# Performance work log

Measured on AMD Instinct MI355X. Metric: run time of the kernel, lower is better.

The kernel has to match this reference:

```python
import jax, jax.numpy as jnp
import numpy as np

LOG_INV_TEMP = float(np.log(1.0 / 0.07))
B, N_IMG, N_GPS, G_DIM = 256, 49, 32, 256


def setup_inputs() -> dict:
    key = jax.random.key(0)
    k1, k2 = jax.random.split(key)
    return {
        "image_g_tokens": jax.random.normal(k1, (B, N_IMG, G_DIM), dtype=jnp.float32),
        "gps_g_tokens": jax.random.normal(k2, (B, N_GPS, G_DIM), dtype=jnp.float32),
        "logit_scale": jnp.asarray(LOG_INV_TEMP, dtype=jnp.float32),
    }


def _l2norm(x, eps=1e-12):
    # matches F.normalize(p=2, dim=-1)
    n = jnp.sqrt(jnp.sum(x * x, axis=-1, keepdims=True))
    return x / jnp.maximum(n, eps)


def _ce(logits, labels):
    # mean cross-entropy with integer labels
    logz = jax.nn.logsumexp(logits, axis=1)
    picked = jnp.take_along_axis(logits, labels[:, None], axis=1)[:, 0]
    return jnp.mean(logz - picked)


def reference(image_g_tokens, gps_g_tokens, logit_scale):
    img = _l2norm(image_g_tokens)   # (B, n, d)
    gps = _l2norm(gps_g_tokens)     # (B, m, d)
    # dist not initialized -> gather is identity, global == local
    scale = jnp.minimum(jnp.exp(logit_scale), 100.0)

    # token-level max-sim: (B, G, n, m) pairwise similarities
    sims_i2g = jnp.einsum('bnd,gmd->bgnm', img, gps)
    sims_g2i = jnp.einsum('bmd,gnd->bgmn', gps, img)
    logits_i2g = jnp.mean(jnp.max(sims_i2g, axis=3), axis=2) * scale  # (B, G)
    logits_g2i = jnp.mean(jnp.max(sims_g2i, axis=3), axis=2) * scale  # (B, G)

    labels = jnp.arange(img.shape[0])
    loss = (_ce(logits_i2g, labels) + _ce(logits_g2i, labels)) / 2.0
    return loss
```

## Files before the change

kernel.cpp:

```cpp
#include <hip/hip_runtime.h>

#define BB   256
#define NIMG 49
#define NGPS 32
#define DIM  256
#define MPAD 64

typedef __attribute__((ext_vector_type(8))) __bf16 bf16x8;
typedef __attribute__((ext_vector_type(4))) float  f32x4;
typedef __attribute__((ext_vector_type(4))) unsigned int u32x4;

__device__ inline unsigned short f2bf(float f) {
  unsigned int u = __float_as_uint(f);
  u += 0x7fff + ((u >> 16) & 1);
  return (unsigned short)(u >> 16);
}

template<int CTRL>
__device__ inline float dppmax(float v) {
  float o = __int_as_float(__builtin_amdgcn_update_dpp(0, __float_as_int(v), CTRL, 0xF, 0xF, true));
  return fmaxf(v, o);
}
template<int CTRL>
__device__ inline float dppadd(float v) {
  float o = __int_as_float(__builtin_amdgcn_update_dpp(0, __float_as_int(v), CTRL, 0xF, 0xF, true));
  return v + o;
}
__device__ inline float max16(float v) {
  v = dppmax<0xB1>(v); v = dppmax<0x4E>(v); v = dppmax<0x141>(v); v = dppmax<0x140>(v);
  return v;
}
__device__ inline float sum16(float v) {
  v = dppadd<0xB1>(v); v = dppadd<0x4E>(v); v = dppadd<0x141>(v); v = dppadd<0x140>(v);
  return v;
}

__global__ __launch_bounds__(256) void norm_kernel(
    const float* __restrict__ img, const float* __restrict__ gps,
    unsigned short* __restrict__ imgS, unsigned short* __restrict__ gpsS)
{
  int w    = (blockIdx.x * 256 + threadIdx.x) >> 6;
  int lane = threadIdx.x & 63;

  f32x4 x = (f32x4){0.f, 0.f, 0.f, 0.f};
  bool isimg; int b = 0, n = 0, g = 0, m = 0;
  if (w < BB * MPAD) {
    isimg = true; b = w >> 6; n = w & 63;
    if (n < NIMG)
      x = *reinterpret_cast<const f32x4*>(img + ((size_t)b * NIMG + n) * DIM + lane * 4);
  } else {
    isimg = false; int t = w - BB * MPAD; g = t >> 5; m = t & 31;
    x = *reinterpret_cast<const f32x4*>(gps + (size_t)t * DIM + lane * 4);
  }

  float ss = x[0]*x[0] + x[1]*x[1] + x[2]*x[2] + x[3]*x[3];
  #pragma unroll
  for (int d = 1; d < 64; d <<= 1) ss += __shfl_xor(ss, d);
  float inv = (ss > 0.f) ? (1.0f / fmaxf(sqrtf(ss), 1e-12f)) : 0.f;

  unsigned int w01 = (unsigned)f2bf(x[0]*inv) | ((unsigned)f2bf(x[1]*inv) << 16);
  unsigned int w23 = (unsigned)f2bf(x[2]*inv) | ((unsigned)f2bf(x[3]*inv) << 16);

  int L = lane;
  unsigned int a0 = __shfl(w01, 2 * L);
  unsigned int a1 = __shfl(w23, 2 * L);
  unsigned int a2 = __shfl(w01, 2 * L + 1);
  unsigned int a3 = __shfl(w23, 2 * L + 1);
  if (L < 32) {
    u32x4 v = {a0, a1, a2, a3};
    unsigned short* dst;
    if (isimg) {
      dst = imgS + (size_t)b * 16384 + L * 512 + n * 8;
    } else {
      int mt = m >> 4, c = m & 15, kc = L >> 2, grp = L & 3;
      dst = gpsS + (size_t)g * 8192 + mt * 4096 + kc * 512 + (grp * 16 + c) * 8;
    }
    *reinterpret_cast<u32x4*>(dst) = v;
  }
}

__global__ __launch_bounds__(256, 3) void pair_kernel(
    const unsigned short* __restrict__ imgS, const unsigned short* __restrict__ gpsS,
    float* __restrict__ i2g, float* __restrict__ g2i)
{
  int tid  = threadIdx.x;
  int wv   = tid >> 6;
  int lane = tid & 63;
  int c    = lane & 15, grp = lane >> 4;
  int b    = blockIdx.x >> 3, gc = blockIdx.x & 7;
  int wvu  = __builtin_amdgcn_readfirstlane(wv);

  __shared__ unsigned short As[MPAD * DIM];

  {
    const unsigned short* src = imgS + (size_t)b * 16384 + lane * 8;
    #pragma unroll
    for (int i = 0; i < 8; ++i) {
      int s = wvu * 8 + i;
      bf16x8 v = *reinterpret_cast<const bf16x8*>(src + s * 512);
      unsigned int rb = lane * 512;
      unsigned int sw = (lane & 7) << 4;
      *reinterpret_cast<bf16x8*>(reinterpret_cast<char*>(As) + ((rb + s * 16) ^ sw)) = v;
    }
  }
  __syncthreads();

  const char* Ab = reinterpret_cast<const char*>(As);
  unsigned int swr   = (c & 7) << 4;
  unsigned int abase = c * 512;

  const unsigned short* gb = gpsS + ((size_t)(gc * 32 + wvu * 8)) * 8192;
  unsigned int lane8 = lane * 8;

  #pragma unroll 1
  for (int st = 0; st < 4; ++st) {
    f32x4 acc[2][2][4];
    #pragma unroll
    for (int g = 0; g < 2; ++g)
      #pragma unroll
      for (int mt = 0; mt < 2; ++mt)
        #pragma unroll
        for (int hf = 0; hf < 4; ++hf)
          acc[g][mt][hf] = (f32x4){0.f, 0.f, 0.f, 0.f};

    #pragma unroll 2
    for (int kc = 0; kc < 8; ++kc) {
      const unsigned short* p = gb + kc * 512 + lane8;
      bf16x8 q00 = *reinterpret_cast<const bf16x8*>(p);
      bf16x8 q01 = *reinterpret_cast<const bf16x8*>(p + 4096);
      bf16x8 q10 = *reinterpret_cast<const bf16x8*>(p + 8192);
      bf16x8 q11 = *reinterpret_cast<const bf16x8*>(p + 12288);
      unsigned int off = ((unsigned)(grp * 16 + kc * 64)) ^ swr;
      const char* ab = Ab + abase + off;
      bf16x8 a0 = *reinterpret_cast<const bf16x8*>(ab);
      bf16x8 a1 = *reinterpret_cast<const bf16x8*>(ab + 8192);
      bf16x8 a2 = *reinterpret_cast<const bf16x8*>(ab + 16384);
      bf16x8 a3 = *reinterpret_cast<const bf16x8*>(ab + 24576);
      acc[0][0][0] = __builtin_amdgcn_mfma_f32_16x16x32_bf16(q00, a0, acc[0][0][0], 0, 0, 0);
      acc[0][0][1] = __builtin_amdgcn_mfma_f32_16x16x32_bf16(q00, a1, acc[0][0][1], 0, 0, 0);
      acc[0][0][2] = __builtin_amdgcn_mfma_f32_16x16x32_bf16(q00, a2, acc[0][0][2], 0, 0, 0);
      acc[0][0][3] = __builtin_amdgcn_mfma_f32_16x16x32_bf16(q00, a3, acc[0][0][3], 0, 0, 0);
      acc[0][1][0] = __builtin_amdgcn_mfma_f32_16x16x32_bf16(q01, a0, acc[0][1][0], 0, 0, 0);
      acc[0][1][1] = __builtin_amdgcn_mfma_f32_16x16x32_bf16(q01, a1, acc[0][1][1], 0, 0, 0);
      acc[0][1][2] = __builtin_amdgcn_mfma_f32_16x16x32_bf16(q01, a2, acc[0][1][2], 0, 0, 0);
      acc[0][1][3] = __builtin_amdgcn_mfma_f32_16x16x32_bf16(q01, a3, acc[0][1][3], 0, 0, 0);
      acc[1][0][0] = __builtin_amdgcn_mfma_f32_16x16x32_bf16(q10, a0, acc[1][0][0], 0, 0, 0);
      acc[1][0][1] = __builtin_amdgcn_mfma_f32_16x16x32_bf16(q10, a1, acc[1][0][1], 0, 0, 0);
      acc[1][0][2] = __builtin_amdgcn_mfma_f32_16x16x32_bf16(q10, a2, acc[1][0][2], 0, 0, 0);
      acc[1][0][3] = __builtin_amdgcn_mfma_f32_16x16x32_bf16(q10, a3, acc[1][0][3], 0, 0, 0);
      acc[1][1][0] = __builtin_amdgcn_mfma_f32_16x16x32_bf16(q11, a0, acc[1][1][0], 0, 0, 0);
      acc[1][1][1] = __builtin_amdgcn_mfma_f32_16x16x32_bf16(q11, a1, acc[1][1][1], 0, 0, 0);
      acc[1][1][2] = __builtin_amdgcn_mfma_f32_16x16x32_bf16(q11, a2, acc[1][1][2], 0, 0, 0);
      acc[1][1][3] = __builtin_amdgcn_mfma_f32_16x16x32_bf16(q11, a3, acc[1][1][3], 0, 0, 0);
    }

    #pragma unroll
    for (int g = 0; g < 2; ++g) {
      float vmax[4];
      #pragma unroll
      for (int hf = 0; hf < 4; ++hf) {
        float m0 = fmaxf(fmaxf(acc[g][0][hf][0], acc[g][0][hf][1]),
                         fmaxf(acc[g][0][hf][2], acc[g][0][hf][3]));
        float m1 = fmaxf(fmaxf(acc[g][1][hf][0], acc[g][1][hf][1]),
                         fmaxf(acc[g][1][hf][2], acc[g][1][hf][3]));
        float vm = fmaxf(m0, m1);
        vm = fmaxf(vm, __shfl_xor(vm, 16));
        vm = fmaxf(vm, __shfl_xor(vm, 32));
        vmax[hf] = vm;
      }
      float s = vmax[0] + vmax[1] + vmax[2] + ((c == 0) ? vmax[3] : 0.0f);
      s = sum16(s);

      float t = 0.f;
      #pragma unroll
      for (int mt = 0; mt < 2; ++mt)
        #pragma unroll
        for (int r = 0; r < 4; ++r) {
          float h3 = (c == 0) ? acc[g][mt][3][r] : -1.0e30f;
          float hm = fmaxf(fmaxf(acc[g][mt][0][r], acc[g][mt][1][r]),
                           fmaxf(acc[g][mt][2][r], h3));
          hm = max16(hm);
          t += hm;
        }
      t += __shfl_xor(t, 16);
      t += __shfl_xor(t, 32);

      if (lane == 0) {
        int gg = gc * 32 + wvu * 8 + st * 2 + g;
        i2g[b * 256 + gg] = s * (1.0f / NIMG);
        g2i[gg * 256 + b] = t * (1.0f / NGPS);
      }
    }
    gb += 16384;
  }
}

__global__ __launch_bounds__(256) void ce_kernel(
    const float* __restrict__ i2g, const float* __restrict__ g2i,
    const float* __restrict__ lsp, float* __restrict__ partial)
{
  int b = blockIdx.x, t = threadIdx.x, lane = t & 63, wv = t >> 6;
  float s = fminf(expf(lsp[0]), 100.0f);
  float v1 = s * i2g[b * 256 + t];
  float v2 = s * g2i[b * 256 + t];

  float m1 = v1, m2 = v2;
  #pragma unroll
  for (int d = 1; d < 64; d <<= 1) {
    m1 = fmaxf(m1, __shfl_xor(m1, d));
    m2 = fmaxf(m2, __shfl_xor(m2, d));
  }
  __shared__ float sm[2][4];
  if (lane == 0) { sm[0][wv] = m1; sm[1][wv] = m2; }
  __syncthreads();
  m1 = fmaxf(fmaxf(sm[0][0], sm[0][1]), fmaxf(sm[0][2], sm[0][3]));
  m2 = fmaxf(fmaxf(sm[1][0], sm[1][1]), fmaxf(sm[1][2], sm[1][3]));

  float e1 = expf(v1 - m1), e2 = expf(v2 - m2);
  #pragma unroll
  for (int d = 1; d < 64; d <<= 1) {
    e1 += __shfl_xor(e1, d);
    e2 += __shfl_xor(e2, d);
  }
  __shared__ float se[2][4];
  if (lane == 0) { se[0][wv] = e1; se[1][wv] = e2; }
  __syncthreads();
  if (t == 0) {
    float S1 = se[0][0] + se[0][1] + se[0][2] + se[0][3];
    float S2 = se[1][0] + se[1][1] + se[1][2] + se[1][3];
    float lse1 = m1 + logf(S1);
    float lse2 = m2 + logf(S2);
    partial[b] = (lse1 - s * i2g[b * 257]) + (lse2 - s * g2i[b * 257]);
  }
}

__global__ __launch_bounds__(256) void finish_kernel(
    const float* __restrict__ partial, float* __restrict__ out)
{
  int t = threadIdx.x, lane = t & 63, wv = t >> 6;
  float v = partial[t];
  #pragma unroll
  for (int d = 1; d < 64; d <<= 1) v += __shfl_xor(v, d);
  __shared__ float sp[4];
  if (lane == 0) sp[wv] = v;
  __syncthreads();
  if (t == 0) out[0] = (sp[0] + sp[1] + sp[2] + sp[3]) * (1.0f / 512.0f);
}

extern "C" void kernel_launch(void* const* d_in, const int* in_sizes, int n_in,
                              void* d_out, int out_size, void* d_ws, size_t ws_size,
                              hipStream_t stream)
{
  const float* img = (const float*)d_in[0];
  const float* gps = (const float*)d_in[1];
  const float* lsp = (const float*)d_in[2];
  float* out = (float*)d_out;
  char* ws = (char*)d_ws;

  unsigned short* imgS = (unsigned short*)(ws);
  unsigned short* gpsS = (unsigned short*)(ws + 8388608);
  float* i2g     = (float*)(ws + 12582912);
  float* g2i     = (float*)(ws + 12845056);
  float* partial = (float*)(ws + 13107200);

  norm_kernel<<<6144, 256, 0, stream>>>(img, gps, imgS, gpsS);
  pair_kernel<<<2048, 256, 0, stream>>>(imgS, gpsS, i2g, g2i);
  ce_kernel<<<256, 256, 0, stream>>>(i2g, g2i, lsp, partial);
  finish_kernel<<<1, 256, 0, stream>>>(partial, out);
}
```

Baseline: 87.35 us.

## Store image tile in MFMA-fragment order in LDS and peel first k-step

Reorders the shared-memory image tile so each lane's MFMA operand is a contiguous 16-byte slot per k-chunk. This removes the XOR swizzle and its address arithmetic and gives linear, conflict-free LDS reads. It also peels the first k iteration to feed zero accumulators directly instead of zero-initialising them, and rewrites the max reductions as three-input max chains so the compiler can emit v_max3. The global load pattern for staging the image changes, which may alter coalescing.

Result: slower. 196.4 us (+124.9%).

```diff
diff --git a/kernel.cpp b/kernel.cpp
--- a/kernel.cpp
+++ b/kernel.cpp
@@ -14,6 +14,10 @@
   unsigned int u = __float_as_uint(f);
   u += 0x7fff + ((u >> 16) & 1);
   return (unsigned short)(u >> 16);
+}
+
+__device__ inline float max3f(float a, float b, float c) {
+  return fmaxf(fmaxf(a, b), c);
 }
 
 template<int CTRL>
@@ -86,28 +90,25 @@
   int tid  = threadIdx.x;
   int wv   = tid >> 6;
   int lane = tid & 63;
-  int c    = lane & 15, grp = lane >> 4;
+  int c    = lane & 15;
   int b    = blockIdx.x >> 3, gc = blockIdx.x & 7;
   int wvu  = __builtin_amdgcn_readfirstlane(wv);
 
-  __shared__ unsigned short As[MPAD * DIM];
+  __shared__ unsigned short As[8 * 4 * 64 * 8];
 
   {
-    const unsigned short* src = imgS + (size_t)b * 16384 + lane * 8;
+    const unsigned short* src = imgS + (size_t)b * 16384;
     #pragma unroll
     for (int i = 0; i < 8; ++i) {
-      int s = wvu * 8 + i;
-      bf16x8 v = *reinterpret_cast<const bf16x8*>(src + s * 512);
-      unsigned int rb = lane * 512;
-      unsigned int sw = (lane & 7) << 4;
-      *reinterpret_cast<bf16x8*>(reinterpret_cast<char*>(As) + ((rb + s * 16) ^ sw)) = v;
-    }
-  }
-  __syncthreads();
-
-  const char* Ab = reinterpret_cast<const char*>(As);
-  unsigned int swr   = (c & 7) << 4;
-  unsigned int abase = c * 512;
+      bf16x8 v = *reinterpret_cast<const bf16x8*>(
+          src + (i * 4 + (lane >> 4)) * 512 + (wvu * 16 + (lane & 15)) * 8);
+      *reinterpret_cast<bf16x8*>(
+          reinterpret_cast<char*>(As) + i * 4096 + wvu * 1024 + lane * 16) = v;
+    }
+  }
+  __syncthreads();
+
+  const char* ab = reinterpret_cast<const char*>(As) + lane * 16;
 
   const unsigned short* gb = gpsS + ((size_t)(gc * 32 + wvu * 8)) * 8192;
   unsigned int lane8 = lane * 8;
@@ -115,27 +116,48 @@
   #pragma unroll 1
   for (int st = 0; st < 4; ++st) {
     f32x4 acc[2][2][4];
-    #pragma unroll
-    for (int g = 0; g < 2; ++g)
-      #pragma unroll
-      for (int mt = 0; mt < 2; ++mt)
-        #pragma unroll
-        for (int hf = 0; hf < 4; ++hf)
-          acc[g][mt][hf] = (f32x4){0.f, 0.f, 0.f, 0.f};
+
+    {
+      const unsigned short* p = gb + lane8;
+      bf16x8 q00 = *reinterpret_cast<const bf16x8*>(p);
+      bf16x8 q01 = *reinterpret_cast<const bf16x8*>(p + 4096);
+      bf16x8 q10 = *reinterpret_cast<const bf16x8*>(p + 8192);
+      bf16x8 q11 = *reinterpret_cast<const bf16x8*>(p + 12288);
+      bf16x8 a0 = *reinterpret_cast<const bf16x8*>(ab);
+      bf16x8 a1 = *reinterpret_cast<const bf16x8*>(ab + 1024);
+      bf16x8 a2 = *reinterpret_cast<const bf16x8*>(ab + 2048);
+      bf16x8 a3 = *reinterpret_cast<const bf16x8*>(ab + 3072);
+      const f32x4 Z = {0.f, 0.f, 0.f, 0.f};
+      acc[0][0][0] = __builtin_amdgcn_mfma_f32_16x16x32_bf16(q00, a0, Z, 0, 0, 0);
+      acc[0][0][1] = __builtin_amdgcn_mfma_f32_16x16x32_bf16(q00, a1, Z, 0, 0, 0);
+      acc[0][0][2] = __builtin_amdgcn_mfma_f32_16x16x32_bf16(q00, a2, Z, 0, 0, 0);
+      acc[0][0][3] = __builtin_amdgcn_mfma_f32_16x16x32_bf16(q00, a3, Z, 0, 0, 0);
+      acc[0][1][0] = __builtin_amdgcn_mfma_f32_16x16x32_bf16(q01, a0, Z, 0, 0, 0);
+      acc[0][1][1] = __builtin_amdgcn_mfma_f32_16x16x32_bf16(q01, a1, Z, 0, 0, 0);
+      acc[0][1][2] = __builtin_amdgcn_mfma_f32_16x16x32_bf16(q01, a2, Z, 0, 0, 0);
+      acc[0][1][3] = __builtin_amdgcn_mfma_f32_16x16x32_bf16(q01, a3, Z, 0, 0, 0);
+      acc[1][0][0] = __builtin_amdgcn_mfma_f32_16x16x32_bf16(q10, a0, Z, 0, 0, 0);
+      acc[1][0][1] = __builtin_amdgcn_mfma_f32_16x16x32_bf16(q10, a1, Z, 0, 0, 0);
+      acc[1][0][2] = __builtin_amdgcn_mfma_f32_16x16x32_bf16(q10, a2, Z, 0, 0, 0);
+      acc[1][0][3] = __builtin_amdgcn_mfma_f32_16x16x32_bf16(q10, a3, Z, 0, 0, 0);
+      acc[1][1][0] = __builtin_amdgcn_mfma_f32_16x16x32_bf16(q11, a0, Z, 0, 0, 0);
+      acc[1][1][1] = __builtin_amdgcn_mfma_f32_16x16x32_bf16(q11, a1, Z, 0, 0, 0);
+      acc[1][1][2] = __builtin_amdgcn_mfma_f32_16x16x32_bf16(q11, a2, Z, 0, 0, 0);
+      acc[1][1][3] = __builtin_amdgcn_mfma_f32_16x16x32_bf16(q11, a3, Z, 0, 0, 0);
+    }
 
     #pragma unroll 2
-    for (int kc = 0; kc < 8; ++kc) {
+    for (int kc = 1; kc < 8; ++kc) {
       const unsigned short* p = gb + kc * 512 + lane8;
       bf16x8 q00 = *reinterpret_cast<const bf16x8*>(p);
       bf16x8 q01 = *reinterpret_cast<const bf16x8*>(p + 4096);
       bf16x8 q10 = *reinterpret_cast<const bf16x8*>(p + 8192);
       bf16x8 q11 = *reinterpret_cast<const bf16x8*>(p + 12288);
-      unsigned int off = ((unsigned)(grp * 16 + kc * 64)) ^ swr;
-      const char* ab = Ab + abase + off;
-      bf16x8 a0 = *reinterpret_cast<const bf16x8*>(ab);
-      bf16x8 a1 = *reinterpret_cast<const bf16x8*>(ab + 8192);
-      bf16x8 a2 = *reinterpret_cast<const bf16x8*>(ab + 16384);
-      bf16x8 a3 = *reinterpret_cast<const bf16x8*>(ab + 24576);
+      const char* ak = ab + kc * 4096;
+      bf16x8 a0 = *reinterpret_cast<const bf16x8*>(ak);
+      bf16x8 a1 = *reinterpret_cast<const bf16x8*>(ak + 1024);
+      bf16x8 a2 = *reinterpret_cast<const bf16x8*>(ak + 2048);
+      bf16x8 a3 = *reinterpret_cast<const bf16x8*>(ak + 3072);
       acc[0][0][0] = __builtin_amdgcn_mfma_f32_16x16x32_bf16(q00, a0, acc[0][0][0], 0, 0, 0);
       acc[0][0][1] = __builtin_amdgcn_mfma_f32_16x16x32_bf16(q00, a1, acc[0][0][1], 0, 0, 0);
       acc[0][0][2] = __builtin_amdgcn_mfma_f32_16x16x32_bf16(q00, a2, acc[0][0][2], 0, 0, 0);
@@ -159,16 +181,15 @@
       float vmax[4];
       #pragma unroll
       for (int hf = 0; hf < 4; ++hf) {
-        float m0 = fmaxf(fmaxf(acc[g][0][hf][0], acc[g][0][hf][1]),
-                         fmaxf(acc[g][0][hf][2], acc[g][0][hf][3]));
-        float m1 = fmaxf(fmaxf(acc[g][1][hf][0], acc[g][1][hf][1]),
-                         fmaxf(acc[g][1][hf][2], acc[g][1][hf][3]));
-        float vm = fmaxf(m0, m1);
+        float vm = fmaxf(max3f(acc[g][0][hf][0], acc[g][0][hf][1], acc[g][0][hf][2]),
+                         max3f(acc[g][0][hf][3], acc[g][1][hf][0], acc[g][1][hf][1]));
+        vm = max3f(vm, acc[g][1][hf][2], acc[g][1][hf][3]);
         vm = fmaxf(vm, __shfl_xor(vm, 16));
         vm = fmaxf(vm, __shfl_xor(vm, 32));
         vmax[hf] = vm;
       }
-      float s = vmax[0] + vmax[1] + vmax[2] + ((c == 0) ? vmax[3] : 0.0f);
+      float s = max3f(0.f, 0.f, 0.f);
+      s = vmax[0] + vmax[1] + vmax[2] + ((c == 0) ? vmax[3] : 0.0f);
       s = sum16(s);
 
       float t = 0.f;
@@ -176,9 +197,8 @@
       for (int mt = 0; mt < 2; ++mt)
         #pragma unroll
         for (int r = 0; r < 4; ++r) {
-          float h3 = (c == 0) ? acc[g][mt][3][r] : -1.0e30f;
-          float hm = fmaxf(fmaxf(acc[g][mt][0][r], acc[g][mt][1][r]),
-                           fmaxf(acc[g][mt][2][r], h3));
+          float h3 = (c == 0) ? acc[g][mt][3][r] : -3.0e38f;
+          float hm = fmaxf(max3f(acc[g][mt][0][r], acc[g][mt][1][r], acc[g][mt][2][r]), h3);
           hm = max16(hm);
           t += hm;
         }
```
